# Kernel tuning notes

Measured on AMD Instinct MI355X. Metric: run time of the kernel, lower is better.

The kernel has to match this reference:

```python
import jax, jax.numpy as jnp
import numpy as np

IN, OUT, WS = 128, 64, 512
B, H, W = 4, 128, 128
GAIN = (2.0 / (1.0 + 0.2 ** 2)) ** 0.5  # util.lrelu_gain for leaky_relu(0.2)
EPS = 1e-8


def up2_bilinear_ac(x):
    # bilinear upsample x2, align_corners=True (torch F.upsample_bilinear semantics)
    _, _, h, w = x.shape
    ys = jnp.linspace(0.0, h - 1.0, 2 * h)
    xs = jnp.linspace(0.0, w - 1.0, 2 * w)
    y0 = jnp.floor(ys).astype(jnp.int32)
    y1 = jnp.minimum(y0 + 1, h - 1)
    wy = (ys - y0).astype(x.dtype)
    x0 = jnp.floor(xs).astype(jnp.int32)
    x1 = jnp.minimum(x0 + 1, w - 1)
    wx = (xs - x0).astype(x.dtype)
    t = x[:, :, y0, :] * (1 - wy)[None, None, :, None] + x[:, :, y1, :] * wy[None, None, :, None]
    return t[:, :, :, x0] * (1 - wx) + t[:, :, :, x1] * wx


def convt3(x, w):
    # torch conv_transpose2d(stride=1, padding=1, k=3) == conv2d with spatially
    # flipped kernel, weight layout [I,O,3,3] -> lax 'IOHW' spec, SAME padding.
    wf = w[:, :, ::-1, ::-1]
    return jax.lax.conv_general_dilated(
        x, wf, (1, 1), ((1, 1), (1, 1)),
        dimension_numbers=('NCHW', 'IOHW', 'NCHW'))


def mod_conv(x, style, w, he):
    # StyleGAN2 modulate + demodulate, expressed in fused activation form:
    # y[b,o] = demod[b,o] * convT(x[b] * style[b,:,None,None], he*W)  (same math
    # as building the per-sample grouped weight tensor in the original).
    wh = w * he                                  # [I,O,3,3]
    wsq = jnp.sum(wh * wh, axis=(2, 3))          # [I,O]
    d = jax.lax.rsqrt(jnp.einsum('bi,io->bo', style * style, wsq) + EPS)  # [B,O]
    y = convt3(x * style[:, :, None, None], wh)
    return y * d[:, :, None, None] * GAIN        # forward also multiplies by gain


def setup_inputs() -> dict:
    key = jax.random.key(0)
    ks = jax.random.split(key, 16)
    f = lambda k, s: jax.random.normal(k, s, dtype=jnp.float32)
    return {
        'x': f(ks[0], (B, IN, H, W)),
        'w': f(ks[1], (B, WS, 1, 1)),
        'conv1_w': f(ks[2], (IN, OUT, 3, 3)),
        'conv2_w': f(ks[3], (OUT, OUT, 3, 3)),
        'bias1': jnp.zeros((1, OUT, 1, 1), jnp.float32),
        'bias2': jnp.zeros((1, OUT, 1, 1), jnp.float32),
        'aaff1_w': f(ks[4], (IN, WS)),
        'aaff1_b': jnp.zeros((IN,), jnp.float32),
        'aaff2_w': f(ks[5], (OUT, WS)),
        'aaff2_b': jnp.zeros((OUT,), jnp.float32),
        'baff1_w': f(ks[6], (OUT,)) * 0.1,
        'baff2_w': f(ks[7], (OUT,)) * 0.1,
        'rgb_w': f(ks[8], (3, OUT)),
        'rgb_b': jnp.zeros((3,), jnp.float32),
        'noise1': f(ks[9], (B, 1, 2 * H, 2 * W)),
        'noise2': f(ks[10], (B, 1, 2 * H, 2 * W)),
    }


def reference(x, w, conv1_w, conv2_w, bias1, bias2, aaff1_w, aaff1_b,
              aaff2_w, aaff2_b, baff1_w, baff2_w, rgb_w, rgb_b,
              noise1, noise2):
    he1 = GAIN / (IN * 9) ** 0.5
    he2 = GAIN / (OUT * 9) ** 0.5
    he_a = 1.0 / WS ** 0.5
    he_rgb = 0.03 / OUT ** 0.5

    xu = up2_bilinear_ac(x)                       # [B,IN,2H,2W]
    wv = w[:, :, 0, 0]                            # [B,WS]

    s1 = jnp.einsum('ow,bw->bo', aaff1_w * he_a, wv) + aaff1_b
    h = mod_conv(xu, s1, conv1_w, he1)
    h = h + noise1 * baff1_w[None, :, None, None] + bias1
    h = jax.nn.leaky_relu(h, 0.2)

    s2 = jnp.einsum('ow,bw->bo', aaff2_w * he_a, wv) + aaff2_b
    h = mod_conv(h, s2, conv2_w, he2)
    h = h + noise2 * baff2_w[None, :, None, None] + bias2
    h = jax.nn.leaky_relu(h, 0.2)

    rgb = jnp.einsum('oc,bchw->bohw', rgb_w * he_rgb, h) + rgb_b[None, :, None, None]
    return (h, rgb)
```

## Files before the change

kernel.cpp:

```cpp
#include <hip/hip_runtime.h>
#include <hip/hip_bf16.h>
#include <math.h>

#define BN 4
#define CIN 128
#define COUT 64
#define WSDIM 512
#define HI 128
#define WI 128
#define HO 256
#define WO 256
#define EPSC 1e-8f
#define GAINC 1.3867504905630728f
#define HE1 (GAINC/33.941125496954285f)
#define HE2 (GAINC/24.0f)
#define SUP (127.0f/255.0f)

typedef __attribute__((ext_vector_type(8))) short s16x8;
typedef __attribute__((ext_vector_type(4))) float f32x4_t;
typedef __attribute__((ext_vector_type(4))) unsigned int u32x4;

static __device__ __forceinline__ float lrelu(float v){ return v > 0.f ? v : 0.2f*v; }
static __device__ __forceinline__ unsigned short bfbits(float v){
  __hip_bfloat16 h = __float2bfloat16(v);
  return *reinterpret_cast<unsigned short*>(&h);
}
static __device__ __forceinline__ unsigned int packbf(float a, float b){
  return (unsigned int)bfbits(a) | ((unsigned int)bfbits(b) << 16);
}

__global__ __launch_bounds__(256) void k_wprep(
    const float* __restrict__ c1w, const float* __restrict__ c2w,
    unsigned short* __restrict__ B1, unsigned short* __restrict__ B2,
    float* __restrict__ wsq1, float* __restrict__ wsq2)
{
  const int g = blockIdx.x, t = threadIdx.x;
  if (g < 144) {
    int cc = g / 36, r = g - cc * 36, k = r >> 2, ot = r & 3;
    for (int e = t; e < 512; e += 256) {
      int l = e >> 3, j = e & 7;
      int c = cc * 32 + (l >> 4) * 8 + j, o = ot * 16 + (l & 15);
      B1[g * 512 + e] = bfbits(c1w[(c * COUT + o) * 9 + (8 - k)] * HE1);
    }
  } else if (g < 288) {
    int g2 = g - 144;
    int cc = g2 / 36, r = g2 - cc * 36, k = r >> 2, ot = r & 3;
    for (int e = t; e < 512; e += 256) {
      int l = e >> 3, j = e & 7;
      int c = cc * 32 + (l >> 4) * 8 + j, o = ot * 16 + (l & 15);
      B2[g2 * 512 + e] = bfbits(c2w[(c * COUT + o) * 9 + (8 - k)] * HE2);
    }
  } else if (g < 292) {
    int base = (g - 288) * 2048;
    #pragma unroll
    for (int i = 0; i < 8; ++i) {
      int idx = base + i * 256 + t;
      const float* wp = c1w + (size_t)idx * 9;
      float s = 0.f;
      #pragma unroll
      for (int k = 0; k < 9; ++k) s += wp[k] * wp[k];
      wsq1[idx] = s;
    }
  } else {
    int base = (g - 292) * 2048;
    #pragma unroll
    for (int i = 0; i < 8; ++i) {
      int idx = base + i * 256 + t;
      const float* wp = c2w + (size_t)idx * 9;
      float s = 0.f;
      #pragma unroll
      for (int k = 0; k < 9; ++k) s += wp[k] * wp[k];
      wsq2[idx] = s;
    }
  }
}

__global__ __launch_bounds__(256) void k_styles(
    const float* __restrict__ w,
    const float* __restrict__ a1w, const float* __restrict__ a1b,
    const float* __restrict__ a2w, const float* __restrict__ a2b,
    const float* __restrict__ wsq1, const float* __restrict__ wsq2,
    float* __restrict__ s1, float* __restrict__ s2,
    float* __restrict__ d1g, float* __restrict__ d2g)
{
  const int b = blockIdx.x, t = threadIdx.x;
  const float he_a = 0.044194173824159216f;
  __shared__ float sh1[CIN];
  __shared__ float sh2[COUT];
  const float* wv = w + b * WSDIM;
  if (t < CIN) {
    float acc = 0.f;
    const float* ap = a1w + t * WSDIM;
    for (int k = 0; k < WSDIM; ++k) acc += ap[k] * wv[k];
    float v = acc * he_a + a1b[t];
    sh1[t] = v; s1[b * CIN + t] = v;
  } else if (t < CIN + COUT) {
    int o = t - CIN;
    float acc = 0.f;
    const float* ap = a2w + o * WSDIM;
    for (int k = 0; k < WSDIM; ++k) acc += ap[k] * wv[k];
    float v = acc * he_a + a2b[o];
    sh2[o] = v; s2[b * COUT + o] = v;
  }
  __syncthreads();
  const int o = t >> 2, p = t & 3;
  float acc = 0.f;
  for (int c = p * 32; c < p * 32 + 32; ++c) acc += sh1[c] * sh1[c] * wsq1[c * COUT + o];
  acc += __shfl_xor(acc, 1); acc += __shfl_xor(acc, 2);
  if (p == 0) d1g[b * COUT + o] = rsqrtf(acc * HE1 * HE1 + EPSC) * GAINC;
  float ac2 = 0.f;
  for (int c = p * 16; c < p * 16 + 16; ++c) ac2 += sh2[c] * sh2[c] * wsq2[c * COUT + o];
  ac2 += __shfl_xor(ac2, 1); ac2 += __shfl_xor(ac2, 2);
  if (p == 0) d2g[b * COUT + o] = rsqrtf(ac2 * HE2 * HE2 + EPSC) * GAINC;
}

__global__ __launch_bounds__(256) void k_up(
    const float* __restrict__ x, const float* __restrict__ s1, unsigned short* __restrict__ XU)
{
  const int bid = blockIdx.x;
  const int swz = (bid & 7) * 128 + (bid >> 3);
  const int b = swz >> 8, yo = swz & 255;
  const int tid = threadIdx.x;
  __shared__ float xs[2][128][36];

  const float fy = yo * SUP;
  const int y0 = (int)fy;
  const float wy = fy - (float)y0;
  const int y1 = min(y0 + 1, HI - 1);

  const float* xb = x + ((size_t)b * CIN << 14);
  unsigned short* outb = XU + (((size_t)b * HO + yo) * WO) * (size_t)CIN;
  const int ch0 = (tid & 3) * 8;

  for (int chunk = 0; chunk < 4; ++chunk) {
    if (chunk) __syncthreads();
    #pragma unroll
    for (int i = 0; i < 2; ++i) {
      int rid = i * 32 + (tid >> 3);
      int c = rid >> 1, r = rid & 1;
      const float* src = xb + (((size_t)(chunk * 32 + c)) << 14) + (r ? y1 : y0) * WI + (tid & 7) * 4;
      #pragma unroll
      for (int k = 0; k < 4; ++k) {
        f32x4_t v = *(const f32x4_t*)(src + k * 32);
        int xp = (tid & 7) * 4 + k * 32;
        xs[r][xp + 0][c] = v[0];
        xs[r][xp + 1][c] = v[1];
        xs[r][xp + 2][c] = v[2];
        xs[r][xp + 3][c] = v[3];
      }
    }
    f32x4_t sA = *(const f32x4_t*)(s1 + b * CIN + chunk * 32 + ch0);
    f32x4_t sB = *(const f32x4_t*)(s1 + b * CIN + chunk * 32 + ch0 + 4);
    __syncthreads();
    #pragma unroll
    for (int pp = 0; pp < 4; ++pp) {
      int pix = pp * 64 + (tid >> 2);
      float fx = pix * SUP;
      int x0 = (int)fx;
      float wx = fx - (float)x0;
      int x1 = min(x0 + 1, WI - 1);

      f32x4_t a0A = *(const f32x4_t*)&xs[0][x0][ch0];
      f32x4_t a1A = *(const f32x4_t*)&xs[0][x1][ch0];
      f32x4_t c0A = *(const f32x4_t*)&xs[1][x0][ch0];
      f32x4_t c1A = *(const f32x4_t*)&xs[1][x1][ch0];
      f32x4_t a0B = *(const f32x4_t*)&xs[0][x0][ch0 + 4];
      f32x4_t a1B = *(const f32x4_t*)&xs[0][x1][ch0 + 4];
      f32x4_t c0B = *(const f32x4_t*)&xs[1][x0][ch0 + 4];
      f32x4_t c1B = *(const f32x4_t*)&xs[1][x1][ch0 + 4];

      float vv[8];
      #pragma unroll
      for (int e = 0; e < 4; ++e) {
        float t0 = a0A[e] + (c0A[e] - a0A[e]) * wy;
        float t1 = a1A[e] + (c1A[e] - a1A[e]) * wy;
        vv[e] = (t0 + (t1 - t0) * wx) * sA[e];
      }
      #pragma unroll
      for (int e = 0; e < 4; ++e) {
        float t0 = a0B[e] + (c0B[e] - a0B[e]) * wy;
        float t1 = a1B[e] + (c1B[e] - a1B[e]) * wy;
        vv[4 + e] = (t0 + (t1 - t0) * wx) * sB[e];
      }
      unsigned int pk[4];
      pk[0] = packbf(vv[0], vv[1]); pk[1] = packbf(vv[2], vv[3]);
      pk[2] = packbf(vv[4], vv[5]); pk[3] = packbf(vv[6], vv[7]);
      *(u32x4*)(outb + (size_t)pix * CIN + chunk * 32 + ch0) = *(u32x4*)pk;
    }
  }
}

__global__ __launch_bounds__(256) void k_conv1(
    const unsigned short* __restrict__ XU, const unsigned short* __restrict__ B1pre,
    const float* __restrict__ noise1, const float* __restrict__ bias1, const float* __restrict__ baff1,
    const float* __restrict__ d1g, const float* __restrict__ s2,
    unsigned short* __restrict__ h1)
{
  const int b = blockIdx.z;
  const int oy0 = blockIdx.y * 16, ox0 = blockIdx.x * 16;
  const int tid = threadIdx.x;
  const int lane = tid & 63, wv = tid >> 6;
  const int lx = lane & 15, lg = lane >> 4;

  __shared__ unsigned int ldsA[324 * 20];

  f32x4_t acc[4][4];
  #pragma unroll
  for (int i = 0; i < 4; ++i)
    #pragma unroll
    for (int j = 0; j < 4; ++j) acc[i][j] = (f32x4_t){0.f, 0.f, 0.f, 0.f};

  const s16x8* Bb = (const s16x8*)B1pre;

  u32x4 rg[6], rg2[6];
  auto LOAD = [&](int cc, u32x4 (&r)[6]) {
    #pragma unroll
    for (int i = 0; i < 6; ++i) {
      int e = i * 256 + tid;
      u32x4 v = {0, 0, 0, 0};
      if (e < 1296) {
        int pos = e >> 2, q = e & 3;
        int ys = pos / 18, xs = pos - ys * 18;
        int yy = oy0 - 1 + ys, xx = ox0 - 1 + xs;
        if (yy >= 0 && yy < HO && xx >= 0 && xx < WO)
          v = *(const u32x4*)(XU + ((((size_t)b * HO + yy) * WO + xx) * CIN + cc * 32 + q * 8));
      }
      r[i] = v;
    }
  };
  auto STORE = [&](u32x4 (&r)[6]) {
    #pragma unroll
    for (int i = 0; i < 6; ++i) {
      int e = i * 256 + tid;
      if (e < 1296) {
        int pos = e >> 2, q = e & 3;
        *(u32x4*)(ldsA + pos * 20 + q * 4) = r[i];
      }
    }
  };

  LOAD(0, rg);
  for (int cc = 0; cc < 4; ++cc) {
    if (cc) __syncthreads();
    STORE(rg);
    if (cc < 3) LOAD(cc + 1, rg2);
    __syncthreads();
    #pragma unroll
    for (int k = 0; k < 9; ++k) {
      const int dy = k / 3, dx = k - 3 * (k / 3);
      s16x8 b0 = Bb[((cc * 9 + k) * 4 + 0) * 64 + lane];
      s16x8 b1 = Bb[((cc * 9 + k) * 4 + 1) * 64 + lane];
      s16x8 b2 = Bb[((cc * 9 + k) * 4 + 2) * 64 + lane];
      s16x8 b3 = Bb[((cc * 9 + k) * 4 + 3) * 64 + lane];
      #pragma unroll
      for (int yi = 0; yi < 4; ++yi) {
        int row = (wv * 4 + yi + dy) * 18 + (lx + dx);
        s16x8 a = *(const s16x8*)((const char*)ldsA + (size_t)row * 80 + lg * 16);
        acc[yi][0] = __builtin_amdgcn_mfma_f32_16x16x32_bf16(a, b0, acc[yi][0], 0, 0, 0);
        acc[yi][1] = __builtin_amdgcn_mfma_f32_16x16x32_bf16(a, b1, acc[yi][1], 0, 0, 0);
        acc[yi][2] = __builtin_amdgcn_mfma_f32_16x16x32_bf16(a, b2, acc[yi][2], 0, 0, 0);
        acc[yi][3] = __builtin_amdgcn_mfma_f32_16x16x32_bf16(a, b3, acc[yi][3], 0, 0, 0);
      }
    }
    if (cc < 3) {
      #pragma unroll
      for (int i = 0; i < 6; ++i) rg[i] = rg2[i];
    }
  }
  #pragma unroll
  for (int yi = 0; yi < 4; ++yi) {
    int y = oy0 + wv * 4 + yi;
    f32x4_t nv = *(const f32x4_t*)(noise1 + (size_t)b * HO * WO + (size_t)y * WO + ox0 + lg * 4);
    #pragma unroll
    for (int ot = 0; ot < 4; ++ot) {
      int o = ot * 16 + lx;
      float d = d1g[b * COUT + o], ba = baff1[o], bi = bias1[o], sv = s2[b * COUT + o];
      #pragma unroll
      for (int jj = 0; jj < 4; ++jj) {
        float v = acc[yi][ot][jj] * d + nv[jj] * ba + bi;
        v = lrelu(v) * sv;
        int xg = ox0 + lg * 4 + jj;
        h1[(((size_t)b * HO + y) * WO + xg) * COUT + o] = bfbits(v);
      }
    }
  }
}

__global__ __launch_bounds__(256) void k_conv2(
    const unsigned short* __restrict__ h1, const unsigned short* __restrict__ B2pre,
    const float* __restrict__ noise2, const float* __restrict__ bias2, const float* __restrict__ baff2,
    const float* __restrict__ d2g, const float* __restrict__ rgbw, const float* __restrict__ rgbb,
    float* __restrict__ hout, float* __restrict__ rgbout)
{
  const int b = blockIdx.z;
  const int oy0 = blockIdx.y * 16, ox0 = blockIdx.x * 16;
  const int tid = threadIdx.x;
  const int lane = tid & 63, wv = tid >> 6;
  const int lx = lane & 15, lg = lane >> 4;

  __shared__ unsigned int ldsA[324 * 20];

  f32x4_t acc[4][4];
  #pragma unroll
  for (int i = 0; i < 4; ++i)
    #pragma unroll
    for (int j = 0; j < 4; ++j) acc[i][j] = (f32x4_t){0.f, 0.f, 0.f, 0.f};

  const s16x8* Bb = (const s16x8*)B2pre;

  u32x4 rg[6], rg2[6];
  auto LOAD = [&](int cc, u32x4 (&r)[6]) {
    #pragma unroll
    for (int i = 0; i < 6; ++i) {
      int e = i * 256 + tid;
      u32x4 v = {0, 0, 0, 0};
      if (e < 1296) {
        int pos = e >> 2, q = e & 3;
        int ys = pos / 18, xs = pos - ys * 18;
        int yy = oy0 - 1 + ys, xx = ox0 - 1 + xs;
        if (yy >= 0 && yy < HO && xx >= 0 && xx < WO)
          v = *(const u32x4*)(h1 + ((((size_t)b * HO + yy) * WO + xx) * COUT + cc * 32 + q * 8));
      }
      r[i] = v;
    }
  };
  auto STORE = [&](u32x4 (&r)[6]) {
    #pragma unroll
    for (int i = 0; i < 6; ++i) {
      int e = i * 256 + tid;
      if (e < 1296) {
        int pos = e >> 2, q = e & 3;
        *(u32x4*)(ldsA + pos * 20 + q * 4) = r[i];
      }
    }
  };

  LOAD(0, rg);
  for (int cc = 0; cc < 2; ++cc) {
    if (cc) __syncthreads();
    STORE(rg);
    if (cc < 1) LOAD(cc + 1, rg2);
    __syncthreads();
    #pragma unroll
    for (int k = 0; k < 9; ++k) {
      const int dy = k / 3, dx = k - 3 * (k / 3);
      s16x8 b0 = Bb[((cc * 9 + k) * 4 + 0) * 64 + lane];
      s16x8 b1 = Bb[((cc * 9 + k) * 4 + 1) * 64 + lane];
      s16x8 b2 = Bb[((cc * 9 + k) * 4 + 2) * 64 + lane];
      s16x8 b3 = Bb[((cc * 9 + k) * 4 + 3) * 64 + lane];
      #pragma unroll
      for (int yi = 0; yi < 4; ++yi) {
        int row = (wv * 4 + yi + dy) * 18 + (lx + dx);
        s16x8 a = *(const s16x8*)((const char*)ldsA + (size_t)row * 80 + lg * 16);
        acc[yi][0] = __builtin_amdgcn_mfma_f32_16x16x32_bf16(a, b0, acc[yi][0], 0, 0, 0);
        acc[yi][1] = __builtin_amdgcn_mfma_f32_16x16x32_bf16(a, b1, acc[yi][1], 0, 0, 0);
        acc[yi][2] = __builtin_amdgcn_mfma_f32_16x16x32_bf16(a, b2, acc[yi][2], 0, 0, 0);
        acc[yi][3] = __builtin_amdgcn_mfma_f32_16x16x32_bf16(a, b3, acc[yi][3], 0, 0, 0);
      }
    }
    if (cc < 1) {
      #pragma unroll
      for (int i = 0; i < 6; ++i) rg[i] = rg2[i];
    }
  }
  const float her = 0.03f / 8.0f;
  #pragma unroll
  for (int yi = 0; yi < 4; ++yi) {
    int y = oy0 + wv * 4 + yi;
    f32x4_t nv = *(const f32x4_t*)(noise2 + (size_t)b * HO * WO + (size_t)y * WO + ox0 + lg * 4);
    float r[3][4];
    #pragma unroll
    for (int ch = 0; ch < 3; ++ch)
      #pragma unroll
      for (int jj = 0; jj < 4; ++jj) r[ch][jj] = 0.f;
    #pragma unroll
    for (int ot = 0; ot < 4; ++ot) {
      int o = ot * 16 + lx;
      float d = d2g[b * COUT + o], ba = baff2[o], bi = bias2[o];
      float w0 = rgbw[o], w1 = rgbw[COUT + o], w2 = rgbw[2 * COUT + o];
      f32x4_t hv;
      #pragma unroll
      for (int jj = 0; jj < 4; ++jj) {
        float v = acc[yi][ot][jj] * d + nv[jj] * ba + bi;
        v = lrelu(v);
        hv[jj] = v;
        r[0][jj] += w0 * v; r[1][jj] += w1 * v; r[2][jj] += w2 * v;
      }
      *(f32x4_t*)(hout + ((size_t)(b * COUT + o) * HO + y) * WO + ox0 + lg * 4) = hv;
    }
    #pragma unroll
    for (int ch = 0; ch < 3; ++ch)
      #pragma unroll
      for (int jj = 0; jj < 4; ++jj) {
        float s = r[ch][jj];
        s += __shfl_xor(s, 1); s += __shfl_xor(s, 2);
        s += __shfl_xor(s, 4); s += __shfl_xor(s, 8);
        r[ch][jj] = s;
      }
    if (lx < 12) {
      float val = 0.f;
      #pragma unroll
      for (int ii = 0; ii < 12; ++ii) if (lx == ii) val = r[ii >> 2][ii & 3];
      int ch = lx >> 2, jj = lx & 3;
      rgbout[(((size_t)(b * 3 + ch)) * HO + y) * WO + ox0 + lg * 4 + jj] = val * her + rgbb[ch];
    }
  }
}

extern "C" void kernel_launch(void* const* d_in, const int* in_sizes, int n_in,
                              void* d_out, int out_size, void* d_ws, size_t ws_size,
                              hipStream_t stream) {
  const float* x      = (const float*)d_in[0];
  const float* w      = (const float*)d_in[1];
  const float* c1w    = (const float*)d_in[2];
  const float* c2w    = (const float*)d_in[3];
  const float* bias1  = (const float*)d_in[4];
  const float* bias2  = (const float*)d_in[5];
  const float* a1w    = (const float*)d_in[6];
  const float* a1b    = (const float*)d_in[7];
  const float* a2w    = (const float*)d_in[8];
  const float* a2b    = (const float*)d_in[9];
  const float* baff1  = (const float*)d_in[10];
  const float* baff2  = (const float*)d_in[11];
  const float* rgbw   = (const float*)d_in[12];
  const float* rgbb   = (const float*)d_in[13];
  const float* noise1 = (const float*)d_in[14];
  const float* noise2 = (const float*)d_in[15];

  const size_t h1_bytes = (size_t)BN * HO * WO * COUT * 2;
  unsigned short* h1 = (unsigned short*)d_ws;
  char* p = (char*)d_ws + h1_bytes;
  float* s1  = (float*)p;               p += BN * CIN * 4;
  float* s2  = (float*)p;               p += BN * COUT * 4;
  float* d1g = (float*)p;               p += BN * COUT * 4;
  float* d2g = (float*)p;               p += BN * COUT * 4;
  float* wsq1 = (float*)p;              p += CIN * COUT * 4;
  float* wsq2 = (float*)p;              p += COUT * COUT * 4;
  unsigned short* B1pre = (unsigned short*)p;  p += 144 * 512 * 2;
  unsigned short* B2pre = (unsigned short*)p;

  unsigned short* XU = (unsigned short*)d_out;
  float* hout   = (float*)d_out;
  float* rgbout = hout + (size_t)BN * COUT * HO * WO;

  k_wprep<<<294, 256, 0, stream>>>(c1w, c2w, B1pre, B2pre, wsq1, wsq2);
  k_styles<<<BN, 256, 0, stream>>>(w, a1w, a1b, a2w, a2b, wsq1, wsq2, s1, s2, d1g, d2g);
  k_up<<<BN * HO, 256, 0, stream>>>(x, s1, XU);
  dim3 grid(WO / 16, HO / 16, BN);
  k_conv1<<<grid, 256, 0, stream>>>(XU, B1pre, noise1, bias1, baff1, d1g, s2, h1);
  k_conv2<<<grid, 256, 0, stream>>>(h1, B2pre, noise2, bias2, baff2, d2g, rgbw, rgbb, hout, rgbout);
}
```

Before: 140.8 us.

## Merge weight-prep and style kernels; double-buffer LDS in conv kernels

Folds the separate weight-squared-norm kernel into the style kernel, which now computes per-channel weight norms inline, so one launch disappears. Both conv kernels switch to a two-slot LDS buffer: each chunk is stored into alternating halves, so one barrier per chunk replaces two and the register staging copy goes away. Launch bounds request 3 blocks per CU. The trade-offs are double the LDS per block, which may cap occupancy, and extra global reads of weights in the style blocks.

After: 202.5 us. +43.8%, slower.

```diff
diff --git a/kernel.cpp b/kernel.cpp
--- a/kernel.cpp
+++ b/kernel.cpp
@@ -29,12 +29,17 @@
   return (unsigned int)bfbits(a) | ((unsigned int)bfbits(b) << 16);
 }
 
-__global__ __launch_bounds__(256) void k_wprep(
-    const float* __restrict__ c1w, const float* __restrict__ c2w,
+__global__ __launch_bounds__(256) void k_prep(
+    const float* __restrict__ w, const float* __restrict__ c1w, const float* __restrict__ c2w,
+    const float* __restrict__ a1w, const float* __restrict__ a1b,
+    const float* __restrict__ a2w, const float* __restrict__ a2b,
     unsigned short* __restrict__ B1, unsigned short* __restrict__ B2,
-    float* __restrict__ wsq1, float* __restrict__ wsq2)
+    float* __restrict__ s1, float* __restrict__ s2,
+    float* __restrict__ d1g, float* __restrict__ d2g)
 {
   const int g = blockIdx.x, t = threadIdx.x;
+  __shared__ float sh1[CIN];
+  __shared__ float sh2[COUT];
   if (g < 144) {
     int cc = g / 36, r = g - cc * 36, k = r >> 2, ot = r & 3;
     for (int e = t; e < 512; e += 256) {
@@ -50,68 +55,47 @@
       int c = cc * 32 + (l >> 4) * 8 + j, o = ot * 16 + (l & 15);
       B2[g2 * 512 + e] = bfbits(c2w[(c * COUT + o) * 9 + (8 - k)] * HE2);
     }
-  } else if (g < 292) {
-    int base = (g - 288) * 2048;
-    #pragma unroll
-    for (int i = 0; i < 8; ++i) {
-      int idx = base + i * 256 + t;
-      const float* wp = c1w + (size_t)idx * 9;
-      float s = 0.f;
-      #pragma unroll
-      for (int k = 0; k < 9; ++k) s += wp[k] * wp[k];
-      wsq1[idx] = s;
-    }
   } else {
-    int base = (g - 292) * 2048;
-    #pragma unroll
-    for (int i = 0; i < 8; ++i) {
-      int idx = base + i * 256 + t;
-      const float* wp = c2w + (size_t)idx * 9;
-      float s = 0.f;
-      #pragma unroll
-      for (int k = 0; k < 9; ++k) s += wp[k] * wp[k];
-      wsq2[idx] = s;
-    }
-  }
-}
-
-__global__ __launch_bounds__(256) void k_styles(
-    const float* __restrict__ w,
-    const float* __restrict__ a1w, const float* __restrict__ a1b,
-    const float* __restrict__ a2w, const float* __restrict__ a2b,
-    const float* __restrict__ wsq1, const float* __restrict__ wsq2,
-    float* __restrict__ s1, float* __restrict__ s2,
-    float* __restrict__ d1g, float* __restrict__ d2g)
-{
-  const int b = blockIdx.x, t = threadIdx.x;
-  const float he_a = 0.044194173824159216f;
-  __shared__ float sh1[CIN];
-  __shared__ float sh2[COUT];
-  const float* wv = w + b * WSDIM;
-  if (t < CIN) {
+    const int b = g - 288;
+    const float he_a = 0.044194173824159216f;
+    const float* wv = w + b * WSDIM;
+    if (t < CIN) {
+      float acc = 0.f;
+      const float* ap = a1w + t * WSDIM;
+      for (int k = 0; k < WSDIM; ++k) acc += ap[k] * wv[k];
+      float v = acc * he_a + a1b[t];
+      sh1[t] = v; s1[b * CIN + t] = v;
+    } else if (t < CIN + COUT) {
+      int o = t - CIN;
+      float acc = 0.f;
+      const float* ap = a2w + o * WSDIM;
+      for (int k = 0; k < WSDIM; ++k) acc += ap[k] * wv[k];
+      float v = acc * he_a + a2b[o];
+      sh2[o] = v; s2[b * COUT + o] = v;
+    }
+    __syncthreads();
+    const int o = t >> 2, p = t & 3;
     float acc = 0.f;
-    const float* ap = a1w + t * WSDIM;
-    for (int k = 0; k < WSDIM; ++k) acc += ap[k] * wv[k];
-    float v = acc * he_a + a1b[t];
-    sh1[t] = v; s1[b * CIN + t] = v;
-  } else if (t < CIN + COUT) {
-    int o = t - CIN;
-    float acc = 0.f;
-    const float* ap = a2w + o * WSDIM;
-    for (int k = 0; k < WSDIM; ++k) acc += ap[k] * wv[k];
-    float v = acc * he_a + a2b[o];
-    sh2[o] = v; s2[b * COUT + o] = v;
-  }
-  __syncthreads();
-  const int o = t >> 2, p = t & 3;
-  float acc = 0.f;
-  for (int c = p * 32; c < p * 32 + 32; ++c) acc += sh1[c] * sh1[c] * wsq1[c * COUT + o];
-  acc += __shfl_xor(acc, 1); acc += __shfl_xor(acc, 2);
-  if (p == 0) d1g[b * COUT + o] = rsqrtf(acc * HE1 * HE1 + EPSC) * GAINC;
-  float ac2 = 0.f;
-  for (int c = p * 16; c < p * 16 + 16; ++c) ac2 += sh2[c] * sh2[c] * wsq2[c * COUT + o];
-  ac2 += __shfl_xor(ac2, 1); ac2 += __shfl_xor(ac2, 2);
-  if (p == 0) d2g[b * COUT + o] = rsqrtf(ac2 * HE2 * HE2 + EPSC) * GAINC;
+    for (int c = p * 32; c < p * 32 + 32; ++c) {
+      const float* wp = c1w + (size_t)(c * COUT + o) * 9;
+      float ws_ = 0.f;
+      #pragma unroll
+      for (int k = 0; k < 9; ++k) ws_ += wp[k] * wp[k];
+      acc += sh1[c] * sh1[c] * ws_;
+    }
+    acc += __shfl_xor(acc, 1); acc += __shfl_xor(acc, 2);
+    if (p == 0) d1g[b * COUT + o] = rsqrtf(acc * HE1 * HE1 + EPSC) * GAINC;
+    float ac2 = 0.f;
+    for (int c = p * 16; c < p * 16 + 16; ++c) {
+      const float* wp = c2w + (size_t)(c * COUT + o) * 9;
+      float ws_ = 0.f;
+      #pragma unroll
+      for (int k = 0; k < 9; ++k) ws_ += wp[k] * wp[k];
+      ac2 += sh2[c] * sh2[c] * ws_;
+    }
+    ac2 += __shfl_xor(ac2, 1); ac2 += __shfl_xor(ac2, 2);
+    if (p == 0) d2g[b * COUT + o] = rsqrtf(ac2 * HE2 * HE2 + EPSC) * GAINC;
+  }
 }
 
 __global__ __launch_bounds__(256) void k_up(
@@ -190,7 +174,7 @@
   }
 }
 
-__global__ __launch_bounds__(256) void k_conv1(
+__global__ __launch_bounds__(256, 3) void k_conv1(
     const unsigned short* __restrict__ XU, const unsigned short* __restrict__ B1pre,
     const float* __restrict__ noise1, const float* __restrict__ bias1, const float* __restrict__ baff1,
     const float* __restrict__ d1g, const float* __restrict__ s2,
@@ -202,7 +186,7 @@
   const int lane = tid & 63, wv = tid >> 6;
   const int lx = lane & 15, lg = lane >> 4;
 
-  __shared__ unsigned int ldsA[324 * 20];
+  __shared__ unsigned int ldsA[2][324 * 20];
 
   f32x4_t acc[4][4];
   #pragma unroll
@@ -212,8 +196,8 @@
 
   const s16x8* Bb = (const s16x8*)B1pre;
 
-  u32x4 rg[6], rg2[6];
-  auto LOAD = [&](int cc, u32x4 (&r)[6]) {
+  u32x4 rg[6];
+  auto LOAD = [&](int cc) {
     #pragma unroll
     for (int i = 0; i < 6; ++i) {
       int e = i * 256 + tid;
@@ -225,26 +209,28 @@
         if (yy >= 0 && yy < HO && xx >= 0 && xx < WO)
           v = *(const u32x4*)(XU + ((((size_t)b * HO + yy) * WO + xx) * CIN + cc * 32 + q * 8));
       }
-      r[i] = v;
+      rg[i] = v;
     }
   };
-  auto STORE = [&](u32x4 (&r)[6]) {
+  auto STORE = [&](unsigned int* buf) {
     #pragma unroll
     for (int i = 0; i < 6; ++i) {
       int e = i * 256 + tid;
       if (e < 1296) {
         int pos = e >> 2, q = e & 3;
-        *(u32x4*)(ldsA + pos * 20 + q * 4) = r[i];
+        *(u32x4*)(buf + pos * 20 + q * 4) = rg[i];
       }
     }
   };
 
-  LOAD(0, rg);
+  LOAD(0);
   for (int cc = 0; cc < 4; ++cc) {
-    if (cc) __syncthreads();
-    STORE(rg);
-    if (cc < 3) LOAD(cc + 1, rg2);
-    __syncthreads();
+    STORE(&ldsA[cc & 1][0]);
+    if (cc < 3) LOAD(cc + 1);
+    asm volatile("s_waitcnt lgkmcnt(0)" ::: "memory");
+    __builtin_amdgcn_s_barrier();
+    asm volatile("" ::: "memory");
+    const unsigned int* buf = &ldsA[cc & 1][0];
     #pragma unroll
     for (int k = 0; k < 9; ++k) {
       const int dy = k / 3, dx = k - 3 * (k / 3);
@@ -255,16 +241,12 @@
       #pragma unroll
       for (int yi = 0; yi < 4; ++yi) {
         int row = (wv * 4 + yi + dy) * 18 + (lx + dx);
-        s16x8 a = *(const s16x8*)((const char*)ldsA + (size_t)row * 80 + lg * 16);
+        s16x8 a = *(const s16x8*)((const char*)buf + (size_t)row * 80 + lg * 16);
         acc[yi][0] = __builtin_amdgcn_mfma_f32_16x16x32_bf16(a, b0, acc[yi][0], 0, 0, 0);
         acc[yi][1] = __builtin_amdgcn_mfma_f32_16x16x32_bf16(a, b1, acc[yi][1], 0, 0, 0);
         acc[yi][2] = __builtin_amdgcn_mfma_f32_16x16x32_bf16(a, b2, acc[yi][2], 0, 0, 0);
         acc[yi][3] = __builtin_amdgcn_mfma_f32_16x16x32_bf16(a, b3, acc[yi][3], 0, 0, 0);
       }
-    }
-    if (cc < 3) {
-      #pragma unroll
-      for (int i = 0; i < 6; ++i) rg[i] = rg2[i];
     }
   }
   #pragma unroll
@@ -286,7 +268,7 @@
   }
 }
 
-__global__ __launch_bounds__(256) void k_conv2(
+__global__ __launch_bounds__(256, 3) void k_conv2(
     const unsigned short* __restrict__ h1, const unsigned short* __restrict__ B2pre,
     const float* __restrict__ noise2, const float* __restrict__ bias2, const float* __restrict__ baff2,
     const float* __restrict__ d2g, const float* __restrict__ rgbw, const float* __restrict__ rgbb,
@@ -298,7 +280,7 @@
   const int lane = tid & 63, wv = tid >> 6;
   const int lx = lane & 15, lg = lane >> 4;
 
-  __shared__ unsigned int ldsA[324 * 20];
+  __shared__ unsigned int ldsA[2][324 * 20];
 
   f32x4_t acc[4][4];
   #pragma unroll
@@ -308,8 +290,8 @@
 
   const s16x8* Bb = (const s16x8*)B2pre;
 
-  u32x4 rg[6], rg2[6];
-  auto LOAD = [&](int cc, u32x4 (&r)[6]) {
+  u32x4 rg[6];
+  auto LOAD = [&](int cc) {
     #pragma unroll
     for (int i = 0; i < 6; ++i) {
       int e = i * 256 + tid;
@@ -321,26 +303,28 @@
         if (yy >= 0 && yy < HO && xx >= 0 && xx < WO)
           v = *(const u32x4*)(h1 + ((((size_t)b * HO + yy) * WO + xx) * COUT + cc * 32 + q * 8));
       }
-      r[i] = v;
+      rg[i] = v;
     }
   };
-  auto STORE = [&](u32x4 (&r)[6]) {
+  auto STORE = [&](unsigned int* buf) {
     #pragma unroll
     for (int i = 0; i < 6; ++i) {
       int e = i * 256 + tid;
       if (e < 1296) {
         int pos = e >> 2, q = e & 3;
-        *(u32x4*)(ldsA + pos * 20 + q * 4) = r[i];
+        *(u32x4*)(buf + pos * 20 + q * 4) = rg[i];
       }
     }
   };
 
-  LOAD(0, rg);
+  LOAD(0);
   for (int cc = 0; cc < 2; ++cc) {
-    if (cc) __syncthreads();
-    STORE(rg);
-    if (cc < 1) LOAD(cc + 1, rg2);
-    __syncthreads();
+    STORE(&ldsA[cc & 1][0]);
+    if (cc < 1) LOAD(cc + 1);
+    asm volatile("s_waitcnt lgkmcnt(0)" ::: "memory");
+    __builtin_amdgcn_s_barrier();
+    asm volatile("" ::: "memory");
+    const unsigned int* buf = &ldsA[cc & 1][0];
     #pragma unroll
     for (int k = 0; k < 9; ++k) {
       const int dy = k / 3, dx = k - 3 * (k / 3);
@@ -351,16 +335,12 @@
       #pragma unroll
       for (int yi = 0; yi < 4; ++yi) {
         int row = (wv * 4 + yi + dy) * 18 + (lx + dx);
-        s16x8 a = *(const s16x8*)((const char*)ldsA + (size_t)row * 80 + lg * 16);
+        s16x8 a = *(const s16x8*)((const char*)buf + (size_t)row * 80 + lg * 16);
         acc[yi][0] = __builtin_amdgcn_mfma_f32_16x16x32_bf16(a, b0, acc[yi][0], 0, 0, 0);
         acc[yi][1] = __builtin_amdgcn_mfma_f32_16x16x32_bf16(a, b1, acc[yi][1], 0, 0, 0);
         acc[yi][2] = __builtin_amdgcn_mfma_f32_16x16x32_bf16(a, b2, acc[yi][2], 0, 0, 0);
         acc[yi][3] = __builtin_amdgcn_mfma_f32_16x16x32_bf16(a, b3, acc[yi][3], 0, 0, 0);
       }
-    }
-    if (cc < 1) {
-      #pragma unroll
-      for (int i = 0; i < 6; ++i) rg[i] = rg2[i];
     }
   }
   const float her = 0.03f / 8.0f;
@@ -434,8 +414,6 @@
   float* s2  = (float*)p;               p += BN * COUT * 4;
   float* d1g = (float*)p;               p += BN * COUT * 4;
   float* d2g = (float*)p;               p += BN * COUT * 4;
-  float* wsq1 = (float*)p;              p += CIN * COUT * 4;
-  float* wsq2 = (float*)p;              p += COUT * COUT * 4;
   unsigned short* B1pre = (unsigned short*)p;  p += 144 * 512 * 2;
   unsigned short* B2pre = (unsigned short*)p;
 
@@ -443,8 +421,7 @@
   float* hout   = (float*)d_out;
   float* rgbout = hout + (size_t)BN * COUT * HO * WO;
 
-  k_wprep<<<294, 256, 0, stream>>>(c1w, c2w, B1pre, B2pre, wsq1, wsq2);
-  k_styles<<<BN, 256, 0, stream>>>(w, a1w, a1b, a2w, a2b, wsq1, wsq2, s1, s2, d1g, d2g);
+  k_prep<<<292, 256, 0, stream>>>(w, c1w, c2w, a1w, a1b, a2w, a2b, B1pre, B2pre, s1, s2, d1g, d2g);
   k_up<<<BN * HO, 256, 0, stream>>>(x, s1, XU);
   dim3 grid(WO / 16, HO / 16, BN);
   k_conv1<<<grid, 256, 0, stream>>>(XU, B1pre, noise1, bias1, baff1, d1g, s2, h1);
```
